# Kernel tuning notes

Hardware: AMD Instinct MI355X
Metric: run time of the kernel (lower is better)

## Reference

```python
import jax, jax.numpy as jnp
import numpy as np

N, S, D, H, L = 1024, 128, 128, 4, 2  # nodes, seq_len, d_model(=heads*C), heads, layers
C = D // H
EPS = 1e-5


def _bn(x, g, b):
    # torch BatchNorm1d training mode applied to [N, D, S]: per-channel stats over (node, seq)
    m = x.mean(axis=(0, 1))
    v = x.var(axis=(0, 1))  # biased variance, matching torch BN normalization
    return (x - m) * jax.lax.rsqrt(v + EPS) * g + b


def _ln(x, g, b):
    m = x.mean(-1, keepdims=True)
    v = x.var(-1, keepdims=True)
    return (x - m) * jax.lax.rsqrt(v + EPS) * g + b


def setup_inputs() -> dict:
    key = jax.random.key(0)
    ks = jax.random.split(key, 16)
    w = lambda k, shape: (jax.random.normal(k, shape, jnp.float32) * 0.05)
    x = jax.random.normal(ks[0], (N, S, D), jnp.float32)
    pad_mask = (jax.random.uniform(ks[1], (N, S, S)) > 0.2).astype(jnp.float32)
    ones = lambda shape: jnp.ones(shape, jnp.float32)
    zeros = lambda shape: jnp.zeros(shape, jnp.float32)
    inp = {
        'x': x, 'pad_mask': pad_mask,
        'lin_in_W': w(ks[2], (D, D)), 'lin_in_b': zeros((D,)),
        'in_bn_g': ones((D,)), 'in_bn_b': zeros((D,)),
        'q_W': w(ks[3], (L, D, D)), 'q_b': zeros((L, D)),
        'q_bn_g': ones((L, D)), 'q_bn_b': zeros((L, D)),
        'k_W': w(ks[4], (L, D, D)), 'k_b': zeros((L, D)),
        'k_bn_g': ones((L, D)), 'k_bn_b': zeros((L, D)),
        'v_W': w(ks[5], (L, D, D)), 'v_b': zeros((L, D)),
        'v_bn_g': ones((L, D)), 'v_bn_b': zeros((L, D)),
        'ln_g': ones((L, D)), 'ln_b': zeros((L, D)),
        'ff_W': w(ks[6], (L, D, D)), 'ff_b': zeros((L, D)),
        'ff_bn_g': ones((L, D)), 'ff_bn_b': zeros((L, D)),
        'skip_W': w(ks[7], (L, D, D)), 'skip_b': zeros((L, D)),
        'skip_bn_g': ones((L, D)), 'skip_bn_b': zeros((L, D)),
    }
    return inp


def reference(x, pad_mask, lin_in_W, lin_in_b, in_bn_g, in_bn_b,
              q_W, q_b, q_bn_g, q_bn_b, k_W, k_b, k_bn_g, k_bn_b,
              v_W, v_b, v_bn_g, v_bn_b, ln_g, ln_b,
              ff_W, ff_b, ff_bn_g, ff_bn_b, skip_W, skip_b, skip_bn_g, skip_bn_b):
    # DetourTransformer.forward: lin_in -> in_bn -> L DetourTransformerLayers -> take seq position 0
    h = _bn(x @ lin_in_W.T + lin_in_b, in_bn_g, in_bn_b)
    mask = pad_mask[:, None]  # [N,1,S,S], multiplicative mask applied BEFORE softmax
    for l in range(L):
        q = _bn(h @ q_W[l].T + q_b[l], q_bn_g[l], q_bn_b[l]).reshape(N, S, H, C)
        k = _bn(h @ k_W[l].T + k_b[l], k_bn_g[l], k_bn_b[l]).reshape(N, S, H, C)
        v = _bn(h @ v_W[l].T + v_b[l], v_bn_g[l], v_bn_b[l]).reshape(N, S, H, C)
        alpha = jnp.einsum('nshc,nthc->nhst', q, k) * mask  # no 1/sqrt(C) scaling in source
        attn = jax.nn.softmax(alpha, axis=-1)
        agg = jnp.einsum('nhst,nthc->nshc', attn, v).reshape(N, S, D)  # concat=True
        out = _ln(agg + h, ln_g[l], ln_b[l])
        ff = _bn(out @ ff_W[l].T + ff_b[l], ff_bn_g[l], ff_bn_b[l])
        out = _ln(out + ff, ln_g[l], ln_b[l])  # same shared LayerNorm params reused
        x_r = _bn(h @ skip_W[l].T + skip_b[l], skip_bn_g[l], skip_bn_b[l])
        h = out + x_r  # root_weight=True, beta=False
    return h[:, 0]
```

## Files before the change

kernel.cpp:

```cpp
#include <hip/hip_runtime.h>
#include <hip/hip_bf16.h>


typedef __attribute__((ext_vector_type(8))) short short8v;
typedef __attribute__((ext_vector_type(16))) float f32x16;

#define NBATCH 1024
#define SEQ    128
#define DIM    128
#define NLAYER 2
#define MTOT   (NBATCH*SEQ)
#define EPSF   1e-5f
#define INV_M  (1.0f/131072.0f)
#define HM32   ((long)MTOT * 32)

__device__ __forceinline__ float bf2f(ushort s) {
  return __uint_as_float(((uint)s) << 16);
}
__device__ __forceinline__ ushort f2bf(float f) {
  uint u = __float_as_uint(f);
  return (ushort)((u + 0x7FFFu + ((u >> 16) & 1u)) >> 16);
}

struct WPtrs { const float* p[11]; };

__global__ __launch_bounds__(256) void prep_w(WPtrs wp, ushort* __restrict__ dst)
{
  const int gid = blockIdx.x * 256 + threadIdx.x;
  const int m = gid >> 11;
  const int rem = gid & 2047;
  const int j = rem >> 4, kc = rem & 15;
  const float* src = wp.p[m];
  float4 a = *(const float4*)(src + j * DIM + kc * 8);
  float4 b = *(const float4*)(src + j * DIM + kc * 8 + 4);
  short8v v;
  v[0] = (short)f2bf(a.x); v[1] = (short)f2bf(a.y);
  v[2] = (short)f2bf(a.z); v[3] = (short)f2bf(a.w);
  v[4] = (short)f2bf(b.x); v[5] = (short)f2bf(b.y);
  v[6] = (short)f2bf(b.z); v[7] = (short)f2bf(b.w);
  const int nt = j >> 5, ln = j & 31;
  *(short8v*)(dst + m * 16384 + kc * 1024 + nt * 256 + ln * 8) = v;
}

__global__ __launch_bounds__(256) void pack_mask(
    const float* __restrict__ mask, uint4* __restrict__ mb)
{
  const int lane = threadIdx.x & 63;
  const int wv   = (blockIdx.x * 256 + threadIdx.x) >> 6;
  const int NW   = gridDim.x * 4;
  for (int row = wv; row < MTOT; row += NW) {
    const float a = mask[(long)row * SEQ + lane];
    const float b = mask[(long)row * SEQ + 64 + lane];
    const unsigned long long lo = __ballot(a != 0.f);
    const unsigned long long hi = __ballot(b != 0.f);
    if (lane == 0) {
      uint4 w;
      w.x = (uint)lo; w.y = (uint)(lo >> 32);
      w.z = (uint)hi; w.w = (uint)(hi >> 32);
      mb[row] = w;
    }
  }
}

template<int OM>
__global__ __launch_bounds__(256, 3) void gemm_one(
    const float* __restrict__ A, const ushort* __restrict__ Wm,
    float* __restrict__ outp, float* __restrict__ stats)
{
  __shared__ float tb[4][32 * 32];
  __shared__ float csum[128], csq[128];
  const int tid = threadIdx.x;
  const int lane = tid & 63, wid = tid >> 6;
  const int hi = lane >> 5, ln = lane & 31;
  const long m0 = (long)blockIdx.x * 128;
  const long arow = m0 + wid * 32 + ln;

  if (tid < 128) { csum[tid] = 0.f; csq[tid] = 0.f; }

  short8v afr[8];
  {
    const float* ar = A + arow * DIM + hi * 8;
#pragma unroll
    for (int kt = 0; kt < 8; ++kt) {
      float4 a0 = *(const float4*)(ar + kt * 16);
      float4 a1 = *(const float4*)(ar + kt * 16 + 4);
      short8v v;
      v[0] = (short)f2bf(a0.x); v[1] = (short)f2bf(a0.y);
      v[2] = (short)f2bf(a0.z); v[3] = (short)f2bf(a0.w);
      v[4] = (short)f2bf(a1.x); v[5] = (short)f2bf(a1.y);
      v[6] = (short)f2bf(a1.z); v[7] = (short)f2bf(a1.w);
      afr[kt] = v;
    }
  }

  f32x16 acc[4];
#pragma unroll
  for (int nt = 0; nt < 4; ++nt)
#pragma unroll
    for (int r = 0; r < 16; ++r) acc[nt][r] = 0.f;

#pragma unroll
  for (int kt = 0; kt < 8; ++kt) {
    const ushort* wb = Wm + (kt * 2 + hi) * 1024 + ln * 8;
#pragma unroll
    for (int nt = 0; nt < 4; ++nt) {
      short8v b = *(const short8v*)(wb + nt * 256);
      acc[nt] = __builtin_amdgcn_mfma_f32_32x32x16_bf16(afr[kt], b, acc[nt], 0, 0, 0);
    }
  }

  float ps[4], pq[4];
#pragma unroll
  for (int nt = 0; nt < 4; ++nt) { ps[nt] = 0.f; pq[nt] = 0.f; }

#pragma unroll
  for (int nt = 0; nt < 4; ++nt) {
#pragma unroll
    for (int r = 0; r < 16; ++r) {
      const float v = acc[nt][r];
      ps[nt] += v; pq[nt] += v * v;
      const int row = (r & 3) + 8 * (r >> 2) + 4 * hi;
      tb[wid][row * 32 + ln] = v;
    }
    if constexpr (OM == 0) {
#pragma unroll
      for (int i = 0; i < 4; ++i) {
        const int row = i * 8 + (lane >> 3);
        float4 v = *(const float4*)&tb[wid][row * 32 + (lane & 7) * 4];
        *(float4*)(outp + (m0 + wid * 32 + row) * DIM + nt * 32 + (lane & 7) * 4) = v;
      }
    } else {
      float* dst = outp + (long)nt * HM32 + (m0 + wid * 32) * 32;
#pragma unroll
      for (int i = 0; i < 4; ++i) {
        float4 v = *(const float4*)&tb[wid][i * 256 + lane * 4];
        *(float4*)(dst + i * 256 + lane * 4) = v;
      }
    }
  }

#pragma unroll
  for (int nt = 0; nt < 4; ++nt) {
    ps[nt] += __shfl_xor(ps[nt], 32);
    pq[nt] += __shfl_xor(pq[nt], 32);
  }
  __syncthreads();
  if (hi == 0) {
#pragma unroll
    for (int nt = 0; nt < 4; ++nt) {
      atomicAdd(&csum[nt * 32 + ln], ps[nt]);
      atomicAdd(&csq[nt * 32 + ln], pq[nt]);
    }
  }
  __syncthreads();
  if (tid < 128) {
    atomicAdd(&stats[tid],       csum[tid]);
    atomicAdd(&stats[128 + tid], csq[tid]);
  }
}

__global__ __launch_bounds__(256, 2) void gemm_qkvs(
    const float* __restrict__ A, const ushort* __restrict__ wbase,
    ushort* __restrict__ o0, ushort* __restrict__ o1,
    ushort* __restrict__ o2, ushort* __restrict__ o3,
    float* __restrict__ st0, float* __restrict__ st1,
    float* __restrict__ st2, float* __restrict__ st3)
{
  __shared__ ushort qtb[4][32 * 32];
  __shared__ float csum[128], csq[128];
  const int tid = threadIdx.x;
  const int lane = tid & 63, wid = tid >> 6;
  const int hi = lane >> 5, ln = lane & 31;
  const long m0 = (long)blockIdx.x * 128;
  const long arow = m0 + wid * 32 + ln;

  if (tid < 128) { csum[tid] = 0.f; csq[tid] = 0.f; }

  short8v afr[8];
  {
    const float* ar = A + arow * DIM + hi * 8;
#pragma unroll
    for (int kt = 0; kt < 8; ++kt) {
      float4 a0 = *(const float4*)(ar + kt * 16);
      float4 a1 = *(const float4*)(ar + kt * 16 + 4);
      short8v v;
      v[0] = (short)f2bf(a0.x); v[1] = (short)f2bf(a0.y);
      v[2] = (short)f2bf(a0.z); v[3] = (short)f2bf(a0.w);
      v[4] = (short)f2bf(a1.x); v[5] = (short)f2bf(a1.y);
      v[6] = (short)f2bf(a1.z); v[7] = (short)f2bf(a1.w);
      afr[kt] = v;
    }
  }

  float ps[4][4], pq[4][4];
#pragma unroll
  for (int w = 0; w < 4; ++w)
#pragma unroll
    for (int nt = 0; nt < 4; ++nt) { ps[w][nt] = 0.f; pq[w][nt] = 0.f; }

#pragma unroll
  for (int w = 0; w < 4; ++w) {
    const ushort* Wm = wbase + ((w < 3) ? w : 4) * 16384;

    f32x16 acc[4];
#pragma unroll
    for (int nt = 0; nt < 4; ++nt)
#pragma unroll
      for (int r = 0; r < 16; ++r) acc[nt][r] = 0.f;
#pragma unroll
    for (int kt = 0; kt < 8; ++kt) {
      const ushort* wb = Wm + (kt * 2 + hi) * 1024 + ln * 8;
#pragma unroll
      for (int nt = 0; nt < 4; ++nt) {
        short8v b = *(const short8v*)(wb + nt * 256);
        acc[nt] = __builtin_amdgcn_mfma_f32_32x32x16_bf16(afr[kt], b, acc[nt], 0, 0, 0);
      }
    }

    ushort* outp = (w == 0) ? o0 : (w == 1) ? o1 : (w == 2) ? o2 : o3;
#pragma unroll
    for (int nt = 0; nt < 4; ++nt) {
#pragma unroll
      for (int r = 0; r < 16; ++r) {
        const float v = acc[nt][r];
        ps[w][nt] += v; pq[w][nt] += v * v;
        const int row = (r & 3) + 8 * (r >> 2) + 4 * hi;
        qtb[wid][row * 32 + ln] = f2bf(v);
      }
      ushort* dst = outp + (long)nt * HM32 + (m0 + wid * 32) * 32;
      short8v v0 = *(const short8v*)&qtb[wid][lane * 8];
      short8v v1 = *(const short8v*)&qtb[wid][512 + lane * 8];
      *(short8v*)(dst + lane * 8)       = v0;
      *(short8v*)(dst + 512 + lane * 8) = v1;
    }
  }

  __syncthreads();
#pragma unroll
  for (int w = 0; w < 4; ++w) {
    float* st = (w == 0) ? st0 : (w == 1) ? st1 : (w == 2) ? st2 : st3;
    float lps[4], lpq[4];
#pragma unroll
    for (int nt = 0; nt < 4; ++nt) {
      lps[nt] = ps[w][nt] + __shfl_xor(ps[w][nt], 32);
      lpq[nt] = pq[w][nt] + __shfl_xor(pq[w][nt], 32);
    }
    if (hi == 0) {
#pragma unroll
      for (int nt = 0; nt < 4; ++nt) {
        atomicAdd(&csum[nt * 32 + ln], lps[nt]);
        atomicAdd(&csq[nt * 32 + ln],  lpq[nt]);
      }
    }
    __syncthreads();
    if (tid < 128) {
      atomicAdd(&st[tid],       csum[tid]);
      atomicAdd(&st[128 + tid], csq[tid]);
      csum[tid] = 0.f; csq[tid] = 0.f;
    }
    __syncthreads();
  }
}

__global__ __launch_bounds__(256) void bn_apply(
    float* __restrict__ x, const float* __restrict__ st,
    const float* __restrict__ g, const float* __restrict__ b)
{
  __shared__ float sc[128], bi[128];
  const int tid = threadIdx.x;
  if (tid < 128) {
    float mean = st[tid] * INV_M;
    float var  = st[128 + tid] * INV_M - mean * mean;
    float s = rsqrtf(var + EPSF) * g[tid];
    sc[tid] = s;
    bi[tid] = b[tid] - mean * s;
  }
  __syncthreads();
  const long total4 = (long)MTOT * DIM / 4;
  for (long i = (long)blockIdx.x * 256 + tid; i < total4; i += (long)gridDim.x * 256) {
    float4 vv = ((const float4*)x)[i];
    const int c = (int)((i * 4) & 127);
    vv.x = vv.x * sc[c + 0] + bi[c + 0];
    vv.y = vv.y * sc[c + 1] + bi[c + 1];
    vv.z = vv.z * sc[c + 2] + bi[c + 2];
    vv.w = vv.w * sc[c + 3] + bi[c + 3];
    ((float4*)x)[i] = vv;
  }
}

__global__ __launch_bounds__(256, 4) void attn_ln(
    const ushort* __restrict__ q, const ushort* __restrict__ k_in,
    const ushort* __restrict__ v_in,
    float* hbuf,
    const uint4* __restrict__ mb,
    const float* __restrict__ qst, const float* __restrict__ kst, const float* __restrict__ vst,
    const float* __restrict__ qg, const float* __restrict__ qbb,
    const float* __restrict__ kg, const float* __restrict__ kbb,
    const float* __restrict__ vg, const float* __restrict__ vbb,
    const float* __restrict__ lng, const float* __restrict__ lnb)
{
  __shared__ ushort Vp[128 * 136];
  __shared__ float qsc[128], qbi[128], ksc[128], kbi[128];
  __shared__ float reds[32][4], redq[32][4];
  __shared__ float2 rmv[32];

  const int tid = threadIdx.x;
  const int lane = tid & 63, hh = tid >> 6;
  const int hi = lane >> 5, ln = lane & 31;
  const int n = blockIdx.x;
  const long nb = (long)n * SEQ;
  const long hbase = (long)hh * HM32 + nb * 32;

  if (tid < 128) {
    const int c = tid;
    float m, v, s;
    m = qst[c] * INV_M; v = qst[128 + c] * INV_M - m * m;
    s = rsqrtf(v + EPSF) * qg[c];  qsc[c] = s; qbi[c] = qbb[c] - m * s;
    m = kst[c] * INV_M; v = kst[128 + c] * INV_M - m * m;
    s = rsqrtf(v + EPSF) * kg[c];  ksc[c] = s; kbi[c] = kbb[c] - m * s;
  }
  const int cg = hh * 32 + ln;
  float vs, vb0;
  {
    float m = vst[cg] * INV_M;
    float v = vst[128 + cg] * INV_M - m * m;
    vs = rsqrtf(v + EPSF) * vg[cg];
    vb0 = vbb[cg] - m * vs;
  }
  const float lgc = lng[cg], lbc = lnb[cg];

#pragma unroll
  for (int it = 0; it < 8; ++it) {
    const int t = it * 16 + (lane >> 2);
    const int c0 = (lane & 3) * 8;
    short8v vv = *(const short8v*)(v_in + hbase + (long)t * 32 + c0);
    const int tl = t & 31;
    const int kt = tl >> 4;
    const int rem = tl & 15;
    const int slot = (t & 96) + (kt << 4) + ((rem >> 2) & 1) * 8 + ((rem & 3) | (((rem >> 3) & 1) << 2));
#pragma unroll
    for (int i = 0; i < 8; ++i) Vp[(hh * 32 + c0 + i) * 136 + slot] = (ushort)vv[i];
  }
  __syncthreads();

  short8v kfr[4][2];
#pragma unroll
  for (int nt = 0; nt < 4; ++nt)
#pragma unroll
    for (int kt = 0; kt < 2; ++kt) {
      short8v raw = *(const short8v*)(k_in + hbase + (long)(nt * 32 + ln) * 32 + kt * 16 + hi * 8);
      short8v f;
#pragma unroll
      for (int i = 0; i < 8; ++i) {
        const int c = hh * 32 + kt * 16 + hi * 8 + i;
        f[i] = (short)f2bf(bf2f((ushort)raw[i]) * ksc[c] + kbi[c]);
      }
      kfr[nt][kt] = f;
    }

  for (int mt = 0; mt < 4; ++mt) {
    short8v qfr[2];
#pragma unroll
    for (int kt = 0; kt < 2; ++kt) {
      short8v raw = *(const short8v*)(q + hbase + (long)(mt * 32 + ln) * 32 + kt * 16 + hi * 8);
      short8v f;
#pragma unroll
      for (int i = 0; i < 8; ++i) {
        const int c = hh * 32 + kt * 16 + hi * 8 + i;
        f[i] = (short)f2bf(bf2f((ushort)raw[i]) * qsc[c] + qbi[c]);
      }
      qfr[kt] = f;
    }

    f32x16 st[4];
#pragma unroll
    for (int nt = 0; nt < 4; ++nt)
#pragma unroll
      for (int r = 0; r < 16; ++r) st[nt][r] = 0.f;
#pragma unroll
    for (int nt = 0; nt < 4; ++nt) {
      st[nt] = __builtin_amdgcn_mfma_f32_32x32x16_bf16(kfr[nt][0], qfr[0], st[nt], 0, 0, 0);
      st[nt] = __builtin_amdgcn_mfma_f32_32x32x16_bf16(kfr[nt][1], qfr[1], st[nt], 0, 0, 0);
    }

    const uint4 bw = mb[nb + mt * 32 + ln];
    float mx = -1e30f;
#pragma unroll
    for (int nt = 0; nt < 4; ++nt) {
      const uint word = (nt == 0) ? bw.x : (nt == 1) ? bw.y : (nt == 2) ? bw.z : bw.w;
#pragma unroll
      for (int r = 0; r < 16; ++r) {
        const int crow = (r & 3) + 8 * (r >> 2) + 4 * hi;
        st[nt][r] = ((word >> crow) & 1u) ? st[nt][r] : 0.f;
        mx = fmaxf(mx, st[nt][r]);
      }
    }
    mx = fmaxf(mx, __shfl_xor(mx, 32));
    float sum = 0.f;
#pragma unroll
    for (int nt = 0; nt < 4; ++nt)
#pragma unroll
      for (int r = 0; r < 16; ++r) {
        const float e = __expf(st[nt][r] - mx);
        st[nt][r] = e;
        sum += e;
      }
    sum += __shfl_xor(sum, 32);
    const float inv = 1.f / sum;

    f32x16 o;
#pragma unroll
    for (int r = 0; r < 16; ++r) o[r] = 0.f;
#pragma unroll
    for (int nt = 0; nt < 4; ++nt) {
#pragma unroll
      for (int kt = 0; kt < 2; ++kt) {
        short8v pa;
#pragma unroll
        for (int j = 0; j < 8; ++j) pa[j] = (short)f2bf(st[nt][kt * 8 + j] * inv);
        short8v vb = *(const short8v*)&Vp[(long)cg * 136 + nt * 32 + kt * 16 + hi * 8];
        o = __builtin_amdgcn_mfma_f32_32x32x16_bf16(pa, vb, o, 0, 0, 0);
      }
    }

    float yv[16];
#pragma unroll
    for (int r = 0; r < 16; ++r) {
      const int sl = (r & 3) + 8 * (r >> 2) + 4 * hi;
      const float hval = hbuf[(nb + mt * 32 + sl) * DIM + cg];
      yv[r] = vs * o[r] + vb0 + hval;
    }

#pragma unroll
    for (int r = 0; r < 16; ++r) {
      float s = yv[r], q2 = yv[r] * yv[r];
      s += __shfl_xor(s, 1);  q2 += __shfl_xor(q2, 1);
      s += __shfl_xor(s, 2);  q2 += __shfl_xor(q2, 2);
      s += __shfl_xor(s, 4);  q2 += __shfl_xor(q2, 4);
      s += __shfl_xor(s, 8);  q2 += __shfl_xor(q2, 8);
      s += __shfl_xor(s, 16); q2 += __shfl_xor(q2, 16);
      if (ln == 0) {
        const int sl = (r & 3) + 8 * (r >> 2) + 4 * hi;
        reds[sl][hh] = s; redq[sl][hh] = q2;
      }
    }
    __syncthreads();
    if (tid < 32) {
      const float s  = reds[tid][0] + reds[tid][1] + reds[tid][2] + reds[tid][3];
      const float q2 = redq[tid][0] + redq[tid][1] + redq[tid][2] + redq[tid][3];
      const float mean = s * (1.f / 128.f);
      const float var  = q2 * (1.f / 128.f) - mean * mean;
      rmv[tid] = make_float2(mean, rsqrtf(var + EPSF));
    }
    __syncthreads();
#pragma unroll
    for (int r = 0; r < 16; ++r) {
      const int sl = (r & 3) + 8 * (r >> 2) + 4 * hi;
      const float2 mr = rmv[sl];
      hbuf[(nb + mt * 32 + sl) * DIM + cg] = (yv[r] - mr.x) * mr.y * lgc + lbc;
    }
  }
}

template <bool FINAL>
__global__ __launch_bounds__(256) void fuse2_k(
    const float* t1, const float* __restrict__ ffr, const ushort* __restrict__ skr,
    const float* __restrict__ fst, const float* __restrict__ sst,
    const float* __restrict__ fg, const float* __restrict__ fb,
    const float* __restrict__ sg, const float* __restrict__ sb,
    const float* __restrict__ lg, const float* __restrict__ lb,
    float* out)
{
  const int lane = threadIdx.x & 63;
  const int c = lane * 2;
  float fs0, fbias0, fs1, fbias1, ss0, sbias0, ss1, sbias1;
  {
    float m0 = fst[c] * INV_M;
    float v0 = fst[128 + c] * INV_M - m0 * m0;
    fs0 = rsqrtf(v0 + EPSF) * fg[c];       fbias0 = fb[c] - m0 * fs0;
    float m1 = fst[c + 1] * INV_M;
    float v1 = fst[128 + c + 1] * INV_M - m1 * m1;
    fs1 = rsqrtf(v1 + EPSF) * fg[c + 1];   fbias1 = fb[c + 1] - m1 * fs1;
    float n0 = sst[c] * INV_M;
    float w0 = sst[128 + c] * INV_M - n0 * n0;
    ss0 = rsqrtf(w0 + EPSF) * sg[c];       sbias0 = sb[c] - n0 * ss0;
    float n1 = sst[c + 1] * INV_M;
    float w1 = sst[128 + c + 1] * INV_M - n1 * n1;
    ss1 = rsqrtf(w1 + EPSF) * sg[c + 1];   sbias1 = sb[c + 1] - n1 * ss1;
  }
  const float lg0 = lg[c], lg1 = lg[c + 1], lb0 = lb[c], lb1 = lb[c + 1];
  const int wid = (blockIdx.x * 256 + threadIdx.x) >> 6;
  const int NW  = gridDim.x * 4;
  const int ROWS = FINAL ? NBATCH : MTOT;
  const long thm = (long)(c >> 5) * HM32;
  for (int r = wid; r < ROWS; r += NW) {
    const long m   = FINAL ? (long)r * SEQ : (long)r;
    const long off = m * DIM + c;
    const long hm  = thm + m * 32 + (c & 31);
    float2 tv = *(const float2*)(t1 + off);
    float2 fv = *(const float2*)(ffr + hm);
    uint sv = *(const uint*)(skr + hm);
    float s0 = bf2f((ushort)(sv & 0xFFFFu)), s1 = bf2f((ushort)(sv >> 16));
    float y0 = tv.x + fv.x * fs0 + fbias0;
    float y1 = tv.y + fv.y * fs1 + fbias1;
    float s = y0 + y1, sq = y0 * y0 + y1 * y1;
#pragma unroll
    for (int o = 32; o; o >>= 1) { s += __shfl_xor(s, o); sq += __shfl_xor(sq, o); }
    const float mean = s * (1.f / 128.f);
    const float var  = sq * (1.f / 128.f) - mean * mean;
    const float rs   = rsqrtf(var + EPSF);
    float o0 = (y0 - mean) * rs * lg0 + lb0 + (s0 * ss0 + sbias0);
    float o1 = (y1 - mean) * rs * lg1 + lb1 + (s1 * ss1 + sbias1);
    const long ooff = FINAL ? ((long)r * DIM + c) : off;
    *(float2*)(out + ooff) = make_float2(o0, o1);
  }
}

extern "C" void kernel_launch(void* const* d_in, const int* in_sizes, int n_in,
                              void* d_out, int out_size, void* d_ws, size_t ws_size,
                              hipStream_t stream)
{
  (void)in_sizes; (void)n_in; (void)out_size; (void)ws_size;
  const float* x    = (const float*)d_in[0];
  const float* mask = (const float*)d_in[1];
  const float* linW = (const float*)d_in[2];
  const float* ing  = (const float*)d_in[4];
  const float* inb  = (const float*)d_in[5];
  const float* qW   = (const float*)d_in[6];
  const float* qg   = (const float*)d_in[8];
  const float* qb   = (const float*)d_in[9];
  const float* kW   = (const float*)d_in[10];
  const float* kg   = (const float*)d_in[12];
  const float* kb   = (const float*)d_in[13];
  const float* vW   = (const float*)d_in[14];
  const float* vg   = (const float*)d_in[16];
  const float* vb   = (const float*)d_in[17];
  const float* lng  = (const float*)d_in[18];
  const float* lnb  = (const float*)d_in[19];
  const float* ffW  = (const float*)d_in[20];
  const float* ffg  = (const float*)d_in[22];
  const float* ffb  = (const float*)d_in[23];
  const float* skW  = (const float*)d_in[24];
  const float* skg  = (const float*)d_in[26];
  const float* skb  = (const float*)d_in[27];

  const long MD = (long)MTOT * DIM;
  float*  stats = (float*)d_ws;
  float*  h     = (float*)d_ws + 4096;
  ushort* qbuf  = (ushort*)(h + MD);
  ushort* kbuf  = qbuf + MD;
  ushort* vbuf  = kbuf + MD;
  ushort* sbuf  = vbuf + MD;
  uint4*  mbits = (uint4*)(sbuf + MD);
  float*  ffbuf = (float*)qbuf;

  ushort* Wsw = (ushort*)d_out;
  hipMemsetAsync(stats, 0, 11 * 256 * sizeof(float), stream);

  WPtrs wp;
  wp.p[0] = linW;
  wp.p[1] = qW;            wp.p[2] = kW;            wp.p[3] = vW;
  wp.p[4] = ffW;           wp.p[5] = skW;
  wp.p[6] = qW + 16384;    wp.p[7] = kW + 16384;    wp.p[8] = vW + 16384;
  wp.p[9] = ffW + 16384;   wp.p[10] = skW + 16384;
  prep_w<<<88, 256, 0, stream>>>(wp, Wsw);
  pack_mask<<<512, 256, 0, stream>>>(mask, mbits);

  gemm_one<0><<<MTOT / 128, 256, 0, stream>>>(x, Wsw, h, stats);
  bn_apply<<<1024, 256, 0, stream>>>(h, stats, ing, inb);

  for (int l = 0; l < NLAYER; ++l) {
    const int poff = l * DIM;
    const ushort* wbase = Wsw + (1 + 5 * l) * 16384;
    float* stq = stats + (1 + 5 * l) * 256;
    float* stk = stats + (2 + 5 * l) * 256;
    float* stv = stats + (3 + 5 * l) * 256;
    float* stf = stats + (4 + 5 * l) * 256;
    float* sts = stats + (5 + 5 * l) * 256;

    gemm_qkvs<<<MTOT / 128, 256, 0, stream>>>(h, wbase, qbuf, kbuf, vbuf, sbuf,
                                              stq, stk, stv, sts);

    attn_ln<<<NBATCH, 256, 0, stream>>>(
        qbuf, kbuf, vbuf, h , mbits,
        stq, stk, stv,
        qg + poff, qb + poff, kg + poff, kb + poff, vg + poff, vb + poff,
        lng + poff, lnb + poff);

    gemm_one<1><<<MTOT / 128, 256, 0, stream>>>(
        h, wbase + 3 * 16384, ffbuf, stf);

    if (l < NLAYER - 1) {
      fuse2_k<false><<<1024, 256, 0, stream>>>(
          h, ffbuf, sbuf, stf, sts,
          ffg + poff, ffb + poff, skg + poff, skb + poff,
          lng + poff, lnb + poff, h );
    } else {
      fuse2_k<true><<<64, 256, 0, stream>>>(
          h, ffbuf, sbuf, stf, sts,
          ffg + poff, ffb + poff, skg + poff, skb + poff,
          lng + poff, lnb + poff, (float*)d_out);
    }
  }
}
```

Measured before the change: 638.8 us.

## Stage GEMM weights in LDS with double-buffered prefetch in QKVS kernel

Both GEMM kernels now copy the bf16 weight matrix into shared memory once per block and read MFMA B-fragments from LDS instead of global memory. In the fused QKV+skip kernel, the next weight matrix is loaded into registers during the current MFMA loop and written to the other LDS buffer afterwards, overlapping the global load with compute. The per-weight stat reductions are also batched so there is a single barrier before the global atomics. This uses about 64 KB more LDS per block in the fused kernel, which may reduce occupancy, and adds a barrier per weight iteration.

```diff
diff --git a/kernel.cpp b/kernel.cpp
--- a/kernel.cpp
+++ b/kernel.cpp
@@ -67,13 +67,18 @@
     const float* __restrict__ A, const ushort* __restrict__ Wm,
     float* __restrict__ outp, float* __restrict__ stats)
 {
-  __shared__ float tb[4][32 * 32];
+  __shared__ ushort Wl[16384];
+  __shared__ float tb[4][1024];
   __shared__ float csum[128], csq[128];
   const int tid = threadIdx.x;
   const int lane = tid & 63, wid = tid >> 6;
   const int hi = lane >> 5, ln = lane & 31;
   const long m0 = (long)blockIdx.x * 128;
   const long arow = m0 + wid * 32 + ln;
+
+#pragma unroll
+  for (int i = 0; i < 8; ++i)
+    ((short8v*)Wl)[i * 256 + tid] = ((const short8v*)Wm)[i * 256 + tid];
 
   if (tid < 128) { csum[tid] = 0.f; csq[tid] = 0.f; }
 
@@ -92,6 +97,7 @@
       afr[kt] = v;
     }
   }
+  __syncthreads();
 
   f32x16 acc[4];
 #pragma unroll
@@ -101,7 +107,7 @@
 
 #pragma unroll
   for (int kt = 0; kt < 8; ++kt) {
-    const ushort* wb = Wm + (kt * 2 + hi) * 1024 + ln * 8;
+    const ushort* wb = Wl + (kt * 2 + hi) * 1024 + ln * 8;
 #pragma unroll
     for (int nt = 0; nt < 4; ++nt) {
       short8v b = *(const short8v*)(wb + nt * 256);
@@ -166,15 +172,19 @@
     float* __restrict__ st0, float* __restrict__ st1,
     float* __restrict__ st2, float* __restrict__ st3)
 {
-  __shared__ ushort qtb[4][32 * 32];
-  __shared__ float csum[128], csq[128];
+  __shared__ ushort wbuf[2][16384];
+  __shared__ ushort qtb[4][1024];
+  __shared__ float csum[4][128], csq[4][128];
   const int tid = threadIdx.x;
   const int lane = tid & 63, wid = tid >> 6;
   const int hi = lane >> 5, ln = lane & 31;
   const long m0 = (long)blockIdx.x * 128;
   const long arow = m0 + wid * 32 + ln;
 
-  if (tid < 128) { csum[tid] = 0.f; csq[tid] = 0.f; }
+  if (tid < 128) {
+#pragma unroll
+    for (int w = 0; w < 4; ++w) { csum[w][tid] = 0.f; csq[w][tid] = 0.f; }
+  }
 
   short8v afr[8];
   {
@@ -192,16 +202,29 @@
     }
   }
 
+#pragma unroll
+  for (int i = 0; i < 8; ++i)
+    ((short8v*)wbuf[0])[i * 256 + tid] = ((const short8v*)wbase)[i * 256 + tid];
+
   float ps[4][4], pq[4][4];
 #pragma unroll
   for (int w = 0; w < 4; ++w)
 #pragma unroll
     for (int nt = 0; nt < 4; ++nt) { ps[w][nt] = 0.f; pq[w][nt] = 0.f; }
 
+  __syncthreads();
+
 #pragma unroll
   for (int w = 0; w < 4; ++w) {
-    const ushort* Wm = wbase + ((w < 3) ? w : 4) * 16384;
-
+    short8v nw[8];
+    if (w < 3) {
+      const int nxt = (w + 1 == 3) ? 4 : (w + 1);
+      const short8v* src = (const short8v*)(wbase + nxt * 16384);
+#pragma unroll
+      for (int i = 0; i < 8; ++i) nw[i] = src[i * 256 + tid];
+    }
+
+    const ushort* wt = wbuf[w & 1];
     f32x16 acc[4];
 #pragma unroll
     for (int nt = 0; nt < 4; ++nt)
@@ -209,12 +232,18 @@
       for (int r = 0; r < 16; ++r) acc[nt][r] = 0.f;
 #pragma unroll
     for (int kt = 0; kt < 8; ++kt) {
-      const ushort* wb = Wm + (kt * 2 + hi) * 1024 + ln * 8;
+      const ushort* wb = wt + (kt * 2 + hi) * 1024 + ln * 8;
 #pragma unroll
       for (int nt = 0; nt < 4; ++nt) {
         short8v b = *(const short8v*)(wb + nt * 256);
         acc[nt] = __builtin_amdgcn_mfma_f32_32x32x16_bf16(afr[kt], b, acc[nt], 0, 0, 0);
       }
+    }
+
+    if (w < 3) {
+      short8v* dst = (short8v*)wbuf[(w + 1) & 1];
+#pragma unroll
+      for (int i = 0; i < 8; ++i) dst[i * 256 + tid] = nw[i];
     }
 
     ushort* outp = (w == 0) ? o0 : (w == 1) ? o1 : (w == 2) ? o2 : o3;
@@ -233,12 +262,11 @@
       *(short8v*)(dst + lane * 8)       = v0;
       *(short8v*)(dst + 512 + lane * 8) = v1;
     }
-  }
-
-  __syncthreads();
+    __syncthreads();
+  }
+
 #pragma unroll
   for (int w = 0; w < 4; ++w) {
-    float* st = (w == 0) ? st0 : (w == 1) ? st1 : (w == 2) ? st2 : st3;
     float lps[4], lpq[4];
 #pragma unroll
     for (int nt = 0; nt < 4; ++nt) {
@@ -248,17 +276,21 @@
     if (hi == 0) {
 #pragma unroll
       for (int nt = 0; nt < 4; ++nt) {
-        atomicAdd(&csum[nt * 32 + ln], lps[nt]);
-        atomicAdd(&csq[nt * 32 + ln],  lpq[nt]);
-      }
-    }
-    __syncthreads();
-    if (tid < 128) {
-      atomicAdd(&st[tid],       csum[tid]);
-      atomicAdd(&st[128 + tid], csq[tid]);
-      csum[tid] = 0.f; csq[tid] = 0.f;
-    }
-    __syncthreads();
+        atomicAdd(&csum[w][nt * 32 + ln], lps[nt]);
+        atomicAdd(&csq[w][nt * 32 + ln],  lpq[nt]);
+      }
+    }
+  }
+  __syncthreads();
+  if (tid < 128) {
+    atomicAdd(&st0[tid],       csum[0][tid]);
+    atomicAdd(&st0[128 + tid], csq[0][tid]);
+    atomicAdd(&st1[tid],       csum[1][tid]);
+    atomicAdd(&st1[128 + tid], csq[1][tid]);
+    atomicAdd(&st2[tid],       csum[2][tid]);
+    atomicAdd(&st2[128 + tid], csq[2][tid]);
+    atomicAdd(&st3[tid],       csum[3][tid]);
+    atomicAdd(&st3[128 + tid], csq[3][tid]);
   }
 }
 
```

New measurement: 514.0 us. -19.5%, faster.
